# Performance work log

Measured on AMD Instinct MI355X. Metric: run time of the kernel, lower is better.

The kernel has to match this reference:

```python
import jax, jax.numpy as jnp
import numpy as np

STATE = 24
ACT = 6
L1 = 100
L2 = 100
CHOL = ACT * (ACT + 1) // 2  # 21
BATCH = 262144


def setup_inputs() -> dict:
    key = jax.random.key(0)
    ks = jax.random.split(key, 9)
    return {
        "states": jax.random.normal(ks[0], (BATCH, STATE), jnp.float32),
        "W1": jax.random.normal(ks[1], (L1, STATE), jnp.float32) * (1.0 / np.sqrt(STATE)),
        "b1": jax.random.normal(ks[2], (L1,), jnp.float32) * 0.01,
        "W2": jax.random.normal(ks[3], (L2, L1), jnp.float32) * (1.0 / np.sqrt(L1)),
        "b2": jax.random.normal(ks[4], (L2,), jnp.float32) * 0.01,
        "Wm": jax.random.normal(ks[5], (ACT, L2), jnp.float32) * (1.0 / np.sqrt(L2)),
        "bm": jax.random.normal(ks[6], (ACT,), jnp.float32) * 0.01,
        "Wc": jax.random.normal(ks[7], (CHOL, L2), jnp.float32) * (1.0 / np.sqrt(L2)),
        "bc": jax.random.normal(ks[8], (CHOL,), jnp.float32) * 0.01,
    }


def reference(states, W1, b1, W2, b2, Wm, bm, Wc, bc):
    # 2-layer MLP backbone
    x = jax.nn.relu(states @ W1.T + b1)          # [B, L1]
    x = jax.nn.relu(x @ W2.T + b2)               # [B, L2]
    mean = jnp.tanh(x @ Wm.T + bm)               # [B, ACT]
    chol_vec = jax.nn.softplus(x @ Wc.T + bc)    # [B, CHOL]
    # Vectorized lower-triangular fill (replaces python double loop + .item()).
    # torch loop fills (i,j) with j<=i in row-major order == tril_indices order.
    rows, cols = jnp.tril_indices(ACT)
    chol = jnp.zeros((states.shape[0], ACT, ACT), chol_vec.dtype).at[:, rows, cols].set(chol_vec)
    return mean, chol
```

## Files before the change

### kernel.cpp

```cpp
#include <hip/hip_runtime.h>
#include <hip/hip_bf16.h>
#include <math.h>

typedef short bf16x8 __attribute__((ext_vector_type(8)));
typedef float f32x4 __attribute__((ext_vector_type(4)));

#define STATE 24
#define L1N 100

#define W1_STRIDE 40
#define K_STRIDE 136
#define W1_OFF 0
#define W2_OFF 4000
#define WH_OFF 17600
#define IMG_U32 10752
#define IMG_BYTES (IMG_U32 * 4)

#define X_HALVES 2176
#define NWAVES 8
#define LDS_BYTES (IMG_BYTES + NWAVES * X_HALVES * 2)

__device__ __constant__ int CHOFF[21] = {0,6,7,12,13,14,18,19,20,21,24,25,26,27,28,30,31,32,33,34,35};
__device__ __constant__ int ZOFF[15]  = {1,2,3,4,5,8,9,10,11,15,16,17,22,23,29};

__device__ inline unsigned short f2bf(float f) {
    union { float f; unsigned u; } v; v.f = f;
    unsigned r = v.u + 0x7FFFu + ((v.u >> 16) & 1u);
    return (unsigned short)(r >> 16);
}
__device__ inline unsigned pkbf(float lo, float hi) {
    __hip_bfloat162 h = __float22bfloat162_rn(float2{lo, hi});
    return *(const unsigned*)&h;
}
__device__ inline float fast_tanh(float x) {
    float e = __builtin_amdgcn_exp2f(x * 2.8853900817779268f);
    return 1.0f - 2.0f * __builtin_amdgcn_rcpf(e + 1.0f);
}
__device__ inline float fast_softplus(float v) {
    float u = __builtin_amdgcn_exp2f(fabsf(v) * -1.4426950408889634f);
    float l = __builtin_amdgcn_logf(1.0f + u) * 0.6931471805599453f;
    return fmaxf(v, 0.0f) + l;
}

__global__ __launch_bounds__(256) void prep_weights(
    const float* __restrict__ W1, const float* __restrict__ W2,
    const float* __restrict__ Wm, const float* __restrict__ Wc,
    unsigned* __restrict__ img)
{
    int i = blockIdx.x * 256 + threadIdx.x;
    if (i >= IMG_U32) return;
    float lo = 0.f, hi = 0.f;
    if (i < 2000) {
        int r = i / 20, k = (i % 20) * 2;
        if (k < STATE)     lo = W1[r * STATE + k];
        if (k + 1 < STATE) hi = W1[r * STATE + k + 1];
    } else if (i < 8800) {
        int j = i - 2000, r = j / 68, k = (j % 68) * 2;
        if (k < L1N)     lo = W2[r * L1N + k];
        if (k + 1 < L1N) hi = W2[r * L1N + k + 1];
    } else if (i < 10636) {
        int j = i - 8800, r = j / 68, k = (j % 68) * 2;
        const float* src = (r < 6) ? (Wm + r * L1N) : (Wc + (r - 6) * L1N);
        if (k < L1N)     lo = src[k];
        if (k + 1 < L1N) hi = src[k + 1];
    }
    img[i] = pkbf(lo, hi);
}

__global__ __launch_bounds__(512, 4) void actor_mfma(
    const float* __restrict__ states,
    const unsigned* __restrict__ img,
    const float* __restrict__ b1, const float* __restrict__ b2,
    const float* __restrict__ bm, const float* __restrict__ bc,
    float* __restrict__ out_mean, float* __restrict__ out_chol)
{
    extern __shared__ __align__(16) unsigned short smem[];
    unsigned short* W1s = smem + W1_OFF;
    unsigned short* W2s = smem + W2_OFF;
    unsigned short* Whs = smem + WH_OFF;
    const int tid = threadIdx.x;

    {
        const uint4* src = (const uint4*)img;
        uint4* dst = (uint4*)smem;
        for (int i = tid; i < IMG_BYTES / 16; i += 512)
            dst[i] = src[i];
    }

    const int wave = tid >> 6, lane = tid & 63;
    unsigned short* XsW = smem + IMG_U32 * 2 + wave * X_HALVES;
    {
        unsigned* xz = (unsigned*)XsW;
        #pragma unroll
        for (int it = 0; it < 5; ++it) {
            int idx = it * 64 + lane;
            int r = idx / 20, s = idx - r * 20;
            xz[r * 68 + 48 + s] = 0u;
        }
    }
    __syncthreads();

    const int q = lane >> 4, c = lane & 15;
    const long rowBase = (long)blockIdx.x * 128 + wave * 16;

    union { bf16x8 v; unsigned u[4]; } af;
    af.u[0] = af.u[1] = af.u[2] = af.u[3] = 0;
    if (q < 3) {
        const float* p = states + (rowBase + c) * STATE + q * 8;
        float4 v0 = *(const float4*)p;
        float4 v1 = *(const float4*)(p + 4);
        af.u[0] = pkbf(v0.x, v0.y); af.u[1] = pkbf(v0.z, v0.w);
        af.u[2] = pkbf(v1.x, v1.y); af.u[3] = pkbf(v1.z, v1.w);
    }
    #pragma unroll
    for (int nt = 0; nt < 7; ++nt) {
        const int n = nt * 16 + c;
        const int cl = n < L1N ? n : L1N - 1;
        bf16x8 bfrag = *(const bf16x8*)&W1s[cl * W1_STRIDE + q * 8];
        const float bias = b1[cl];
        f32x4 acc = {bias, bias, bias, bias};
        acc = __builtin_amdgcn_mfma_f32_16x16x32_bf16(af.v, bfrag, acc, 0, 0, 0);
        if (n < L1N) {
            #pragma unroll
            for (int i = 0; i < 4; ++i)
                XsW[(q * 4 + i) * K_STRIDE + n] = f2bf(fmaxf(acc[i], 0.f));
        }
    }

    bf16x8 a2[4];
    #pragma unroll
    for (int ks = 0; ks < 4; ++ks)
        a2[ks] = *(const bf16x8*)&XsW[c * K_STRIDE + ks * 32 + q * 8];
    f32x4 acc2[7];
    #pragma unroll
    for (int nt = 0; nt < 7; ++nt) {
        const int n = nt * 16 + c;
        const float bias = b2[n < L1N ? n : L1N - 1];
        acc2[nt] = (f32x4){bias, bias, bias, bias};
    }
    #pragma unroll
    for (int ks = 0; ks < 4; ++ks) {
        #pragma unroll
        for (int nt = 0; nt < 7; ++nt) {
            const int cl = (nt * 16 + c) < L1N ? (nt * 16 + c) : L1N - 1;
            bf16x8 bfrag = *(const bf16x8*)&W2s[cl * K_STRIDE + ks * 32 + q * 8];
            acc2[nt] = __builtin_amdgcn_mfma_f32_16x16x32_bf16(a2[ks], bfrag, acc2[nt], 0, 0, 0);
        }
    }
    #pragma unroll
    for (int nt = 0; nt < 7; ++nt) {
        const int n = nt * 16 + c;
        if (n < L1N) {
            #pragma unroll
            for (int i = 0; i < 4; ++i)
                XsW[(q * 4 + i) * K_STRIDE + n] = f2bf(fmaxf(acc2[nt][i], 0.f));
        }
    }

    bf16x8 a3[4];
    #pragma unroll
    for (int ks = 0; ks < 4; ++ks)
        a3[ks] = *(const bf16x8*)&XsW[c * K_STRIDE + ks * 32 + q * 8];
    const float bias0 = (c < 6) ? bm[c] : bc[c - 6];
    const float bias1 = bc[(c + 10) < 21 ? (c + 10) : 20];
    f32x4 acc3[2] = {{bias0, bias0, bias0, bias0}, {bias1, bias1, bias1, bias1}};
    #pragma unroll
    for (int ks = 0; ks < 4; ++ks) {
        #pragma unroll
        for (int ht = 0; ht < 2; ++ht) {
            const int cl = (ht * 16 + c) < 27 ? (ht * 16 + c) : 26;
            bf16x8 bfrag = *(const bf16x8*)&Whs[cl * K_STRIDE + ks * 32 + q * 8];
            acc3[ht] = __builtin_amdgcn_mfma_f32_16x16x32_bf16(a3[ks], bfrag, acc3[ht], 0, 0, 0);
        }
    }

    if (c < 6) {
        #pragma unroll
        for (int i = 0; i < 4; ++i)
            out_mean[(rowBase + q * 4 + i) * 6 + c] = fast_tanh(acc3[0][i]);
    } else {
        const int off = CHOFF[c - 6];
        #pragma unroll
        for (int i = 0; i < 4; ++i)
            out_chol[(rowBase + q * 4 + i) * 36 + off] = fast_softplus(acc3[0][i]);
    }
    if (c < 11) {
        const int off = CHOFF[c + 10];
        #pragma unroll
        for (int i = 0; i < 4; ++i)
            out_chol[(rowBase + q * 4 + i) * 36 + off] = fast_softplus(acc3[1][i]);
    }
    #pragma unroll
    for (int it = 0; it < 4; ++it) {
        int idx = it * 64 + lane;
        if (idx < 240) {
            int r = idx / 15, o = ZOFF[idx - r * 15];
            out_chol[(rowBase + r) * 36 + o] = 0.f;
        }
    }
}

extern "C" void kernel_launch(void* const* d_in, const int* in_sizes, int n_in,
                              void* d_out, int out_size, void* d_ws, size_t ws_size,
                              hipStream_t stream) {
    const float* states = (const float*)d_in[0];
    const float* W1 = (const float*)d_in[1];
    const float* b1 = (const float*)d_in[2];
    const float* W2 = (const float*)d_in[3];
    const float* b2 = (const float*)d_in[4];
    const float* Wm = (const float*)d_in[5];
    const float* bm = (const float*)d_in[6];
    const float* Wc = (const float*)d_in[7];
    const float* bc = (const float*)d_in[8];

    const int batch = in_sizes[0] / STATE;
    float* out_mean = (float*)d_out;
    float* out_chol = out_mean + (size_t)batch * 6;
    unsigned* img = (unsigned*)d_ws;

    hipFuncSetAttribute((const void*)actor_mfma,
                        hipFuncAttributeMaxDynamicSharedMemorySize, LDS_BYTES);

    prep_weights<<<(IMG_U32 + 255) / 256, 256, 0, stream>>>(W1, W2, Wm, Wc, img);
    actor_mfma<<<batch / 128, 512, LDS_BYTES, stream>>>(states, img, b1, b2, bm, bc,
                                                        out_mean, out_chol);
}
```

Baseline: 120.0 us.

## Make MLP kernel persistent with 32-row waves and prefetched states

Replaces the one-tile-per-block launch with a fixed grid of 512 persistent blocks of 256 threads that loop over 128-row tiles. The weight image is copied into LDS once per block instead of once per tile. Each wave now handles 32 rows, so every weight fragment loaded from LDS feeds two MFMAs. States for the next tile are loaded before the current tile is computed. The operand order is swapped so activations are written to LDS as packed 4-element stores, and biases and output offsets are hoisted out of the loop. In exchange it uses more registers and has fewer waves in flight, which may hurt latency hiding and output store throughput.

Result: slower. 124.0 us (+3.3%).

```diff
diff --git a/kernel.cpp b/kernel.cpp
--- a/kernel.cpp
+++ b/kernel.cpp
@@ -3,6 +3,7 @@
 #include <math.h>
 
 typedef short bf16x8 __attribute__((ext_vector_type(8)));
+typedef short bf16x4 __attribute__((ext_vector_type(4)));
 typedef float f32x4 __attribute__((ext_vector_type(4)));
 
 #define STATE 24
@@ -15,10 +16,13 @@
 #define WH_OFF 17600
 #define IMG_U32 10752
 #define IMG_BYTES (IMG_U32 * 4)
-
-#define X_HALVES 2176
-#define NWAVES 8
+#define IMG_HALVES (IMG_U32 * 2)
+
+#define X_HALVES (32 * K_STRIDE)
+#define NWAVES 4
 #define LDS_BYTES (IMG_BYTES + NWAVES * X_HALVES * 2)
+
+#define GRID 512
 
 __device__ __constant__ int CHOFF[21] = {0,6,7,12,13,14,18,19,20,21,24,25,26,27,28,30,31,32,33,34,35};
 __device__ __constant__ int ZOFF[15]  = {1,2,3,4,5,8,9,10,11,15,16,17,22,23,29};
@@ -67,135 +71,178 @@
     img[i] = pkbf(lo, hi);
 }
 
-__global__ __launch_bounds__(512, 4) void actor_mfma(
+__global__ __launch_bounds__(256, 2) void actor_mfma(
     const float* __restrict__ states,
     const unsigned* __restrict__ img,
     const float* __restrict__ b1, const float* __restrict__ b2,
     const float* __restrict__ bm, const float* __restrict__ bc,
-    float* __restrict__ out_mean, float* __restrict__ out_chol)
+    float* __restrict__ out_mean, float* __restrict__ out_chol, int ntiles)
 {
     extern __shared__ __align__(16) unsigned short smem[];
+    const int tid = threadIdx.x;
+    {
+        const uint4* src = (const uint4*)img;
+        uint4* dst = (uint4*)smem;
+        for (int i = tid; i < IMG_BYTES / 16; i += 256) dst[i] = src[i];
+    }
+    const int wave = tid >> 6, lane = tid & 63, q = lane >> 4, c = lane & 15;
     unsigned short* W1s = smem + W1_OFF;
     unsigned short* W2s = smem + W2_OFF;
     unsigned short* Whs = smem + WH_OFF;
-    const int tid = threadIdx.x;
-
+    unsigned short* X   = smem + IMG_HALVES + wave * X_HALVES;
     {
-        const uint4* src = (const uint4*)img;
-        uint4* dst = (uint4*)smem;
-        for (int i = tid; i < IMG_BYTES / 16; i += 512)
-            dst[i] = src[i];
-    }
-
-    const int wave = tid >> 6, lane = tid & 63;
-    unsigned short* XsW = smem + IMG_U32 * 2 + wave * X_HALVES;
-    {
-        unsigned* xz = (unsigned*)XsW;
-        #pragma unroll
-        for (int it = 0; it < 5; ++it) {
+        unsigned* xz = (unsigned*)X;
+        #pragma unroll
+        for (int it = 0; it < 10; ++it) {
+            int i = it * 64 + lane;
+            int r = i / 20, s = i - r * 20;
+            xz[r * 68 + 48 + s] = 0u;
+        }
+    }
+    __syncthreads();
+
+    f32x4 bias1[7], bias2[7];
+    #pragma unroll
+    for (int nt = 0; nt < 7; ++nt)
+        #pragma unroll
+        for (int i = 0; i < 4; ++i) {
+            int f = nt * 16 + q * 4 + i; f = f < L1N ? f : L1N - 1;
+            bias1[nt][i] = b1[f]; bias2[nt][i] = b2[f];
+        }
+    f32x4 bias3[2]; int eoff[8], ekind[8];
+    #pragma unroll
+    for (int ht = 0; ht < 2; ++ht)
+        #pragma unroll
+        for (int i = 0; i < 4; ++i) {
+            int f = ht * 16 + q * 4 + i, e = ht * 4 + i;
+            if (f < 6)       { bias3[ht][i] = bm[f];     eoff[e] = f;            ekind[e] = 0; }
+            else if (f < 27) { bias3[ht][i] = bc[f - 6]; eoff[e] = CHOFF[f - 6]; ekind[e] = 1; }
+            else             { bias3[ht][i] = 0.f;       eoff[e] = 0;            ekind[e] = -1; }
+        }
+    int zoff_[8], zrow_[8];
+    #pragma unroll
+    for (int it = 0; it < 8; ++it) {
+        int idx = it * 64 + lane;
+        int r = idx / 15;
+        zrow_[it] = r; zoff_[it] = ZOFF[idx - r * 15 < 15 ? idx - r * 15 : 0];
+    }
+
+    float4 sv[4];
+    auto loadStates = [&](int tt) {
+        if (tt < ntiles && q < 3) {
+            long rb = (long)tt * 128 + wave * 32;
+            #pragma unroll
+            for (int u = 0; u < 2; ++u) {
+                const float* p = states + (rb + u * 16 + c) * STATE + q * 8;
+                sv[u * 2]     = *(const float4*)p;
+                sv[u * 2 + 1] = *(const float4*)(p + 4);
+            }
+        }
+    };
+    loadStates(blockIdx.x);
+
+    for (int t = blockIdx.x; t < ntiles; t += GRID) {
+        const long rowW = (long)t * 128 + wave * 32;
+
+        union { bf16x8 v; unsigned u[4]; } sb[2];
+        #pragma unroll
+        for (int u = 0; u < 2; ++u) {
+            if (q < 3) {
+                sb[u].u[0] = pkbf(sv[u*2].x,   sv[u*2].y);
+                sb[u].u[1] = pkbf(sv[u*2].z,   sv[u*2].w);
+                sb[u].u[2] = pkbf(sv[u*2+1].x, sv[u*2+1].y);
+                sb[u].u[3] = pkbf(sv[u*2+1].z, sv[u*2+1].w);
+            } else sb[u].u[0] = sb[u].u[1] = sb[u].u[2] = sb[u].u[3] = 0u;
+        }
+        loadStates(t + GRID);
+
+        #pragma unroll
+        for (int nt = 0; nt < 7; ++nt) {
+            int wr = nt * 16 + c; wr = wr < L1N ? wr : L1N - 1;
+            bf16x8 wf = *(const bf16x8*)&W1s[wr * W1_STRIDE + q * 8];
+            #pragma unroll
+            for (int u = 0; u < 2; ++u) {
+                f32x4 acc = bias1[nt];
+                acc = __builtin_amdgcn_mfma_f32_16x16x32_bf16(wf, sb[u].v, acc, 0, 0, 0);
+                if (nt * 16 + q * 4 < L1N) {
+                    bf16x4 pk;
+                    #pragma unroll
+                    for (int i = 0; i < 4; ++i) pk[i] = (short)f2bf(fmaxf(acc[i], 0.f));
+                    *(bf16x4*)&X[(u * 16 + c) * K_STRIDE + nt * 16 + q * 4] = pk;
+                }
+            }
+        }
+
+        bf16x8 ab[2][4];
+        #pragma unroll
+        for (int u = 0; u < 2; ++u)
+            #pragma unroll
+            for (int ks = 0; ks < 4; ++ks)
+                ab[u][ks] = *(const bf16x8*)&X[(u * 16 + c) * K_STRIDE + ks * 32 + q * 8];
+        f32x4 acc2[2][7];
+        #pragma unroll
+        for (int u = 0; u < 2; ++u)
+            #pragma unroll
+            for (int nt = 0; nt < 7; ++nt) acc2[u][nt] = bias2[nt];
+        #pragma unroll
+        for (int ks = 0; ks < 4; ++ks)
+            #pragma unroll
+            for (int nt = 0; nt < 7; ++nt) {
+                int wr = nt * 16 + c; wr = wr < L1N ? wr : L1N - 1;
+                bf16x8 wf = *(const bf16x8*)&W2s[wr * K_STRIDE + ks * 32 + q * 8];
+                acc2[0][nt] = __builtin_amdgcn_mfma_f32_16x16x32_bf16(wf, ab[0][ks], acc2[0][nt], 0, 0, 0);
+                acc2[1][nt] = __builtin_amdgcn_mfma_f32_16x16x32_bf16(wf, ab[1][ks], acc2[1][nt], 0, 0, 0);
+            }
+        #pragma unroll
+        for (int nt = 0; nt < 7; ++nt)
+            if (nt * 16 + q * 4 < L1N)
+                #pragma unroll
+                for (int u = 0; u < 2; ++u) {
+                    bf16x4 pk;
+                    #pragma unroll
+                    for (int i = 0; i < 4; ++i) pk[i] = (short)f2bf(fmaxf(acc2[u][nt][i], 0.f));
+                    *(bf16x4*)&X[(u * 16 + c) * K_STRIDE + nt * 16 + q * 4] = pk;
+                }
+
+        bf16x8 ab3[2][4];
+        #pragma unroll
+        for (int u = 0; u < 2; ++u)
+            #pragma unroll
+            for (int ks = 0; ks < 4; ++ks)
+                ab3[u][ks] = *(const bf16x8*)&X[(u * 16 + c) * K_STRIDE + ks * 32 + q * 8];
+        f32x4 acc3[2][2];
+        #pragma unroll
+        for (int u = 0; u < 2; ++u) { acc3[u][0] = bias3[0]; acc3[u][1] = bias3[1]; }
+        #pragma unroll
+        for (int ks = 0; ks < 4; ++ks)
+            #pragma unroll
+            for (int ht = 0; ht < 2; ++ht) {
+                int wr = ht * 16 + c; wr = wr < 27 ? wr : 26;
+                bf16x8 wf = *(const bf16x8*)&Whs[wr * K_STRIDE + ks * 32 + q * 8];
+                acc3[0][ht] = __builtin_amdgcn_mfma_f32_16x16x32_bf16(wf, ab3[0][ks], acc3[0][ht], 0, 0, 0);
+                acc3[1][ht] = __builtin_amdgcn_mfma_f32_16x16x32_bf16(wf, ab3[1][ks], acc3[1][ht], 0, 0, 0);
+            }
+
+        #pragma unroll
+        for (int u = 0; u < 2; ++u) {
+            const long r = rowW + u * 16 + c;
+            float* mrow = out_mean + r * 6;
+            float* crow = out_chol + r * 36;
+            #pragma unroll
+            for (int ht = 0; ht < 2; ++ht)
+                #pragma unroll
+                for (int i = 0; i < 4; ++i) {
+                    int e = ht * 4 + i;
+                    float v = acc3[u][ht][i];
+                    if (ekind[e] == 0)      mrow[eoff[e]] = fast_tanh(v);
+                    else if (ekind[e] == 1) crow[eoff[e]] = fast_softplus(v);
+                }
+        }
+        #pragma unroll
+        for (int it = 0; it < 8; ++it) {
             int idx = it * 64 + lane;
-            int r = idx / 20, s = idx - r * 20;
-            xz[r * 68 + 48 + s] = 0u;
-        }
-    }
-    __syncthreads();
-
-    const int q = lane >> 4, c = lane & 15;
-    const long rowBase = (long)blockIdx.x * 128 + wave * 16;
-
-    union { bf16x8 v; unsigned u[4]; } af;
-    af.u[0] = af.u[1] = af.u[2] = af.u[3] = 0;
-    if (q < 3) {
-        const float* p = states + (rowBase + c) * STATE + q * 8;
-        float4 v0 = *(const float4*)p;
-        float4 v1 = *(const float4*)(p + 4);
-        af.u[0] = pkbf(v0.x, v0.y); af.u[1] = pkbf(v0.z, v0.w);
-        af.u[2] = pkbf(v1.x, v1.y); af.u[3] = pkbf(v1.z, v1.w);
-    }
-    #pragma unroll
-    for (int nt = 0; nt < 7; ++nt) {
-        const int n = nt * 16 + c;
-        const int cl = n < L1N ? n : L1N - 1;
-        bf16x8 bfrag = *(const bf16x8*)&W1s[cl * W1_STRIDE + q * 8];
-        const float bias = b1[cl];
-        f32x4 acc = {bias, bias, bias, bias};
-        acc = __builtin_amdgcn_mfma_f32_16x16x32_bf16(af.v, bfrag, acc, 0, 0, 0);
-        if (n < L1N) {
-            #pragma unroll
-            for (int i = 0; i < 4; ++i)
-                XsW[(q * 4 + i) * K_STRIDE + n] = f2bf(fmaxf(acc[i], 0.f));
-        }
-    }
-
-    bf16x8 a2[4];
-    #pragma unroll
-    for (int ks = 0; ks < 4; ++ks)
-        a2[ks] = *(const bf16x8*)&XsW[c * K_STRIDE + ks * 32 + q * 8];
-    f32x4 acc2[7];
-    #pragma unroll
-    for (int nt = 0; nt < 7; ++nt) {
-        const int n = nt * 16 + c;
-        const float bias = b2[n < L1N ? n : L1N - 1];
-        acc2[nt] = (f32x4){bias, bias, bias, bias};
-    }
-    #pragma unroll
-    for (int ks = 0; ks < 4; ++ks) {
-        #pragma unroll
-        for (int nt = 0; nt < 7; ++nt) {
-            const int cl = (nt * 16 + c) < L1N ? (nt * 16 + c) : L1N - 1;
-            bf16x8 bfrag = *(const bf16x8*)&W2s[cl * K_STRIDE + ks * 32 + q * 8];
-            acc2[nt] = __builtin_amdgcn_mfma_f32_16x16x32_bf16(a2[ks], bfrag, acc2[nt], 0, 0, 0);
-        }
-    }
-    #pragma unroll
-    for (int nt = 0; nt < 7; ++nt) {
-        const int n = nt * 16 + c;
-        if (n < L1N) {
-            #pragma unroll
-            for (int i = 0; i < 4; ++i)
-                XsW[(q * 4 + i) * K_STRIDE + n] = f2bf(fmaxf(acc2[nt][i], 0.f));
-        }
-    }
-
-    bf16x8 a3[4];
-    #pragma unroll
-    for (int ks = 0; ks < 4; ++ks)
-        a3[ks] = *(const bf16x8*)&XsW[c * K_STRIDE + ks * 32 + q * 8];
-    const float bias0 = (c < 6) ? bm[c] : bc[c - 6];
-    const float bias1 = bc[(c + 10) < 21 ? (c + 10) : 20];
-    f32x4 acc3[2] = {{bias0, bias0, bias0, bias0}, {bias1, bias1, bias1, bias1}};
-    #pragma unroll
-    for (int ks = 0; ks < 4; ++ks) {
-        #pragma unroll
-        for (int ht = 0; ht < 2; ++ht) {
-            const int cl = (ht * 16 + c) < 27 ? (ht * 16 + c) : 26;
-            bf16x8 bfrag = *(const bf16x8*)&Whs[cl * K_STRIDE + ks * 32 + q * 8];
-            acc3[ht] = __builtin_amdgcn_mfma_f32_16x16x32_bf16(a3[ks], bfrag, acc3[ht], 0, 0, 0);
-        }
-    }
-
-    if (c < 6) {
-        #pragma unroll
-        for (int i = 0; i < 4; ++i)
-            out_mean[(rowBase + q * 4 + i) * 6 + c] = fast_tanh(acc3[0][i]);
-    } else {
-        const int off = CHOFF[c - 6];
-        #pragma unroll
-        for (int i = 0; i < 4; ++i)
-            out_chol[(rowBase + q * 4 + i) * 36 + off] = fast_softplus(acc3[0][i]);
-    }
-    if (c < 11) {
-        const int off = CHOFF[c + 10];
-        #pragma unroll
-        for (int i = 0; i < 4; ++i)
-            out_chol[(rowBase + q * 4 + i) * 36 + off] = fast_softplus(acc3[1][i]);
-    }
-    #pragma unroll
-    for (int it = 0; it < 4; ++it) {
-        int idx = it * 64 + lane;
-        if (idx < 240) {
-            int r = idx / 15, o = ZOFF[idx - r * 15];
-            out_chol[(rowBase + r) * 36 + o] = 0.f;
+            if (idx < 480)
+                out_chol[(rowW + zrow_[it]) * 36 + zoff_[it]] = 0.f;
         }
     }
 }
@@ -222,6 +269,7 @@
                         hipFuncAttributeMaxDynamicSharedMemorySize, LDS_BYTES);
 
     prep_weights<<<(IMG_U32 + 255) / 256, 256, 0, stream>>>(W1, W2, Wm, Wc, img);
-    actor_mfma<<<batch / 128, 512, LDS_BYTES, stream>>>(states, img, b1, b2, bm, bc,
-                                                        out_mean, out_chol);
-}
+    const int ntiles = batch / 128;
+    actor_mfma<<<GRID, 256, LDS_BYTES, stream>>>(states, img, b1, b2, bm, bc,
+                                                 out_mean, out_chol, ntiles);
+}
```
